# Optimization experiments

Hardware: AMD Instinct MI355X
Metric: run time of the kernel (lower is better)

Reference implementation:

```python
import jax, jax.numpy as jnp
import numpy as np

WS = 8          # window size (8x8)
HEADS = 8
DIM_HEAD = 28
SCALE = DIM_HEAD ** -0.5


def _window_partition(t, ws=WS):
    # [b, H, W, c] -> [b, n_windows, ws*ws, c]
    b, H, W, c = t.shape
    t = t.reshape(b, H // ws, ws, W // ws, ws, c)
    t = t.transpose(0, 1, 3, 2, 4, 5)
    return t.reshape(b, (H // ws) * (W // ws), ws * ws, c)


def _window_reverse(t, H, W, ws=WS):
    # [b, n_windows, ws*ws, c] -> [b, H, W, c]
    b = t.shape[0]
    c = t.shape[-1]
    t = t.reshape(b, H // ws, W // ws, ws, ws, c)
    t = t.transpose(0, 1, 3, 2, 4, 5)
    return t.reshape(b, H, W, c)


def _heads_split(t, nh):
    # [b, n, mm, (nh*d)] -> [b, n, nh, mm, d]
    b, n, mm, cd = t.shape
    return t.reshape(b, n, mm, nh, cd // nh).transpose(0, 1, 3, 2, 4)


def setup_inputs() -> dict:
    key = jax.random.key(0)
    ks = jax.random.split(key, 6)
    b, H, W, c = 128, 32, 32, 224
    inner = DIM_HEAD * HEADS  # 224
    return {
        "x": jax.random.normal(ks[0], (b, H, W, c), jnp.float32),
        "Wq": jax.random.normal(ks[1], (c, inner), jnp.float32) * (c ** -0.5),
        "Wkv": jax.random.normal(ks[2], (c, 2 * inner), jnp.float32) * (c ** -0.5),
        "Wout": jax.random.normal(ks[3], (inner, c), jnp.float32) * (inner ** -0.5),
        "bout": jnp.zeros((c,), jnp.float32),
        "pos_emb1": jax.random.normal(ks[4], (1, 1, HEADS // 2, WS * WS, WS * WS), jnp.float32),
        "pos_emb2": jax.random.normal(ks[5], (1, 1, HEADS // 2, 16, 16), jnp.float32),
    }


def reference(x, Wq, Wkv, Wout, bout, pos_emb1, pos_emb2):
    b, H, W, c = x.shape
    nh = HEADS // 2  # heads per branch

    q = x @ Wq                       # [b,H,W,224]
    kv = x @ Wkv
    k, v = jnp.split(kv, 2, axis=-1)

    half = c // 2
    q1, q2 = q[..., :half], q[..., half:]
    k1, k2 = k[..., :half], k[..., half:]
    v1, v2 = v[..., :half], v[..., half:]

    # ----- local branch: attention within each 8x8 window -----
    q1 = _heads_split(_window_partition(q1), nh) * SCALE  # [b,n,nh,64,d]
    k1 = _heads_split(_window_partition(k1), nh)
    v1 = _heads_split(_window_partition(v1), nh)
    sim1 = jnp.einsum('bnhid,bnhjd->bnhij', q1, k1) + pos_emb1
    attn1 = jax.nn.softmax(sim1, axis=-1)
    out1 = jnp.einsum('bnhij,bnhjd->bnhid', attn1, v1)    # [b,n,nh,64,d]
    bN = out1.shape[1]
    out1 = out1.transpose(0, 1, 3, 2, 4).reshape(b, bN, WS * WS, half)

    # ----- global branch: attention across windows (same in-window position) -----
    def part_global(t):
        t = _window_partition(t)                 # [b,n,mm,half]
        t = t.transpose(0, 2, 1, 3)              # [b,mm,n,half]
        return _heads_split(t, nh)               # [b,mm,nh,n,d]
    q2 = part_global(q2) * SCALE
    k2 = part_global(k2)
    v2 = part_global(v2)
    sim2 = jnp.einsum('bnhid,bnhjd->bnhij', q2, k2) + pos_emb2
    attn2 = jax.nn.softmax(sim2, axis=-1)
    out2 = jnp.einsum('bnhij,bnhjd->bnhid', attn2, v2)    # [b,mm,nh,n,d]
    out2 = out2.transpose(0, 1, 3, 2, 4).reshape(b, WS * WS, bN, half)
    out2 = out2.transpose(0, 2, 1, 3)                     # [b,n,mm,half]

    out = jnp.concatenate([out1, out2], axis=-1)          # [b,n,mm,c]
    out = out @ Wout + bout
    return _window_reverse(out, H, W)
```

## Files before the change

kernel.cpp:

```cpp
#include <hip/hip_runtime.h>
#include <stdint.h>

typedef short s8v __attribute__((ext_vector_type(8)));
typedef float f4v __attribute__((ext_vector_type(4)));
typedef unsigned short u16;

#define MFMA16(a, b, c) __builtin_amdgcn_mfma_f32_16x16x32_bf16(a, b, c, 0, 0, 0)
#define SCALE 0.1889822365046136f

__device__ __forceinline__ u16 f2bf(float f) {
  union { float f; uint32_t u; } v;
  v.f = f;
  uint32_t u = v.u;
  u += 0x7fffu + ((u >> 16) & 1u);
  return (u16)(u >> 16);
}

__device__ __forceinline__ void gld_lds16(const void* g, void* l) {
  __builtin_amdgcn_global_load_lds(
      (const __attribute__((address_space(1))) void*)g,
      (__attribute__((address_space(3))) void*)l, 16, 0, 0);
}

__global__ void prep_kernel(const float* __restrict__ Wq,
                            const float* __restrict__ Wkv,
                            const float* __restrict__ Wout,
                            u16* __restrict__ wqkvt,
                            u16* __restrict__ woutt) {
  const int gsz = gridDim.x * blockDim.x;
  const int gt = blockIdx.x * blockDim.x + threadIdx.x;
  for (int i = gt; i < 768 * 224; i += gsz) {
    const int n = i / 224, k = i - n * 224;
    float v = 0.f;
    if (n < 224) v = Wq[k * 224 + n];
    else if (n < 672) v = Wkv[k * 448 + (n - 224)];
    wqkvt[i] = f2bf(v);
  }
  for (int i = gt; i < 256 * 224; i += gsz) {
    const int n = i / 224, k = i - n * 224;
    const float v = (n < 224) ? Wout[k * 224 + n] : 0.f;
    woutt[i] = f2bf(v);
  }
}

template <int A_F32, int OUT_F32, int NTILES>
__global__ __launch_bounds__(256) void gemm_af(const void* __restrict__ Ap,
                                               const u16* __restrict__ Bt,
                                               void* __restrict__ Cp,
                                               const float* __restrict__ bias,
                                               int Nvalid, int ldc) {
  extern __shared__ u16 smem[];
  u16* As  = smem;
  u16* Bs0 = smem + 28672;
  u16* Bs1 = smem + 32768;
  const int tid = threadIdx.x;
  const int wave = tid >> 6, lane = tid & 63;
  const int c16 = lane & 15, g = lane >> 4;
  const int m0 = blockIdx.x * 128;
  const int wm = wave & 1, wn = wave >> 1;

  const int fbw = wave * 1024 + lane * 16;
  const int brow0 = fbw >> 6, bcol0 = (fbw & 63) >> 1;

#define STAGE_B(ntile, ktile, bufp)                                            \
  do {                                                                         \
    char* bb = (char*)((bufp) ? Bs1 : Bs0) + wave * 1024;                      \
    const u16* src =                                                           \
        Bt + (size_t)((ntile) * 128 + brow0) * 224 + (ktile) * 32 + bcol0;     \
    gld_lds16(src, bb);                                                        \
    gld_lds16(src + (size_t)64 * 224, bb + 4096);                              \
  } while (0)

  STAGE_B(0, 0, 0);
  if (NTILES * 7 > 1) STAGE_B(0, 1, 1);

  if (A_F32) {
    const float* Af = (const float*)Ap + (size_t)m0 * 224;
#pragma unroll
    for (int rnd = 0; rnd < 28; ++rnd) {
      const int e0 = rnd * 1024 + tid * 4;
      const float4 v = *(const float4*)(Af + e0);
      ushort4 o;
      o.x = f2bf(v.x); o.y = f2bf(v.y); o.z = f2bf(v.z); o.w = f2bf(v.w);
      *(ushort4*)(As + e0) = o;
    }
  } else {
    for (int rnd = 0; rnd < 14; ++rnd) {
      const int fb = rnd * 4096 + fbw;
      const int row = fb / 448;
      const int off = fb - row * 448;
      gld_lds16((const u16*)Ap + (size_t)(m0 + row) * 224 + (off >> 1),
                (char*)As + rnd * 4096 + wave * 1024);
    }
  }

  __syncthreads();

  for (int nt = 0; nt < NTILES; ++nt) {
    f4v acc[4][4] = {};
    for (int kt = 0; kt < 7; ++kt) {
      const int t = nt * 7 + kt;
      const u16* Bs = (t & 1) ? Bs1 : Bs0;
      s8v af[4], bf[4];
      for (int tt = 0; tt < 4; ++tt)
        af[tt] = *(const s8v*)&As[(wm * 64 + tt * 16 + c16) * 224 + kt * 32 + g * 8];
      for (int tt = 0; tt < 4; ++tt)
        bf[tt] = *(const s8v*)&Bs[(wn * 64 + tt * 16 + c16) * 32 + g * 8];
      for (int i = 0; i < 4; ++i)
        for (int j = 0; j < 4; ++j)
          acc[i][j] = MFMA16(af[i], bf[j], acc[i][j]);
      __syncthreads();
      const int ns = t + 2;
      if (ns < NTILES * 7) {
        const int nnt = ns / 7;
        STAGE_B(nnt, ns - nnt * 7, t & 1);
      }
    }
    const int n0 = nt * 128;
    for (int i = 0; i < 4; ++i) {
      const int rowb = m0 + wm * 64 + i * 16 + g * 4;
      for (int j = 0; j < 4; ++j) {
        const int col = n0 + wn * 64 + j * 16 + c16;
        if (col < Nvalid) {
          if (OUT_F32) {
            const float bz = bias[col];
            for (int r = 0; r < 4; ++r)
              ((float*)Cp)[(size_t)(rowb + r) * ldc + col] = acc[i][j][r] + bz;
          } else {
            for (int r = 0; r < 4; ++r)
              ((u16*)Cp)[(size_t)(rowb + r) * ldc + col] = f2bf(acc[i][j][r]);
          }
        }
      }
    }
  }
#undef STAGE_B
}

__device__ __forceinline__ void attn_local_body(u16* sm, int blk, int tid,
                                                const u16* __restrict__ qkv,
                                                const float* __restrict__ pos1,
                                                u16* __restrict__ attn) {
  u16* qs = sm;
  u16* ks = sm + 8192;
  u16* vt = sm + 18432;
  u16* pm = sm;
  const int b = blk >> 4, win = blk & 15;
  const int wy = win >> 2, wx = win & 3;
  const int base_s = (b * 32 + wy * 8) * 32 + wx * 8;
#pragma unroll
  for (int m = 0; m < 14; ++m) {
    const int idx = m * 256 + tid;
    const int q7 = idx / 7;
    const int c4 = idx - q7 * 7;
    const int t = q7 & 63, h = (q7 >> 6) & 3, mtx = q7 >> 8;
    const int s = base_s + (t >> 3) * 32 + (t & 7);
    const ushort4 v = *(const ushort4*)(qkv + (size_t)s * 672 + mtx * 224 + h * 28 + c4 * 4);
    *(ushort4*)((mtx ? ks : qs) + (h * 64 + t) * 32 + c4 * 4) = v;
  }
#pragma unroll
  for (int m = 0; m < 2; ++m) {
    const int idx = m * 256 + tid;
    const int mtx = idx >> 8;
    const int h = (idx >> 6) & 3, t = idx & 63;
    const ushort4 z = {0, 0, 0, 0};
    *(ushort4*)((mtx ? ks : qs) + (h * 64 + t) * 32 + 28) = z;
  }
  {
    const int t = tid & 63, wq = tid >> 6;
    const int s = base_s + (t >> 3) * 32 + (t & 7);
    const u16* vrow = qkv + (size_t)s * 672 + 448 + wq * 28;
    u16* vcolbase = vt + (wq * 32) * 72 + t;
#pragma unroll
    for (int c4 = 0; c4 < 7; ++c4) {
      const ushort4 v = *(const ushort4*)(vrow + c4 * 4);
      u16* col = vcolbase + (c4 * 4) * 72;
      col[0] = v.x; col[72] = v.y; col[144] = v.z; col[216] = v.w;
    }
  }
  __syncthreads();
  const int h = tid >> 6, lane = tid & 63;
  const int c16 = lane & 15, g = lane >> 4;
  s8v af[4], bf[4];
  for (int t = 0; t < 4; ++t) af[t] = *(const s8v*)&qs[(h * 64 + t * 16 + c16) * 32 + g * 8];
  for (int t = 0; t < 4; ++t) bf[t] = *(const s8v*)&ks[(h * 64 + t * 16 + c16) * 32 + g * 8];
  const f4v fz = {0.f, 0.f, 0.f, 0.f};
  f4v sc[4][4];
  for (int i = 0; i < 4; ++i)
    for (int j = 0; j < 4; ++j)
      sc[i][j] = MFMA16(af[i], bf[j], fz);
  float lrow[4][4];
  const float* ph = pos1 + h * 4096;
  for (int i = 0; i < 4; ++i) {
    for (int r = 0; r < 4; ++r) {
      const int irow = i * 16 + g * 4 + r;
      float mx = -1e30f;
      for (int j = 0; j < 4; ++j) {
        const float v = sc[i][j][r] * SCALE + ph[irow * 64 + j * 16 + c16];
        sc[i][j][r] = v;
        mx = fmaxf(mx, v);
      }
      for (int d = 1; d < 16; d <<= 1) mx = fmaxf(mx, __shfl_xor(mx, d, 64));
      float sum = 0.f;
      for (int j = 0; j < 4; ++j) {
        const float e = __expf(sc[i][j][r] - mx);
        sc[i][j][r] = e;
        sum += e;
      }
      for (int d = 1; d < 16; d <<= 1) sum += __shfl_xor(sum, d, 64);
      lrow[i][r] = sum;
    }
  }
  __syncthreads();
  for (int i = 0; i < 4; ++i)
    for (int r = 0; r < 4; ++r) {
      const int irow = i * 16 + g * 4 + r;
      for (int j = 0; j < 4; ++j)
        pm[(h * 64 + irow) * 72 + j * 16 + c16] = f2bf(sc[i][j][r]);
    }
  f4v o[4][2] = {};
  for (int kk = 0; kk < 2; ++kk) {
    s8v ap[4], bv[2];
    for (int t = 0; t < 4; ++t)
      ap[t] = *(const s8v*)&pm[(h * 64 + t * 16 + c16) * 72 + kk * 32 + g * 8];
    for (int t = 0; t < 2; ++t)
      bv[t] = *(const s8v*)&vt[(h * 32 + t * 16 + c16) * 72 + kk * 32 + g * 8];
    for (int i = 0; i < 4; ++i)
      for (int j = 0; j < 2; ++j)
        o[i][j] = MFMA16(ap[i], bv[j], o[i][j]);
  }
  for (int i = 0; i < 4; ++i)
    for (int r = 0; r < 4; ++r) {
      const int irow = i * 16 + g * 4 + r;
      const int s = base_s + (irow >> 3) * 32 + (irow & 7);
      const float inv = 1.f / lrow[i][r];
      for (int j = 0; j < 2; ++j) {
        const int d = j * 16 + c16;
        if (d < 28)
          attn[(size_t)s * 224 + h * 28 + d] = f2bf(o[i][j][r] * inv);
      }
    }
}

__device__ __forceinline__ void attn_global_body(u16* smg, int blk, int tid,
                                                 const u16* __restrict__ qkv,
                                                 const float* __restrict__ pos2,
                                                 u16* __restrict__ attn) {
  u16* qs = smg;
  u16* ks = smg + 8192;
  u16* vt = smg + 16384;
  u16* p2 = smg + 24608;
  const int b = blk >> 4, ig = blk & 15;
#pragma unroll
  for (int m = 0; m < 14; ++m) {
    const int idx = m * 256 + tid;
    const int q7 = idx / 7;
    const int d4 = idx - q7 * 7;
    const int hq = q7 & 3, row = (q7 >> 2) & 63, seg = q7 >> 8;
    const int w = row >> 4, j = row & 15;
    const int ii = ig * 4 + w;
    const int y = ii >> 3, x = ii & 7;
    const int s = (b * 32 + (j >> 2) * 8 + y) * 32 + (j & 3) * 8 + x;
    const ushort4 v =
        *(const ushort4*)(qkv + (size_t)s * 672 + 112 + seg * 224 + hq * 28 + d4 * 4);
    *(ushort4*)((seg ? ks : qs) + ((w * 4 + hq) * 16 + j) * 32 + hq * 0 + d4 * 4) = v;
  }
  {
    const int j = tid & 15, w = (tid >> 4) & 3, wq = tid >> 6;
    const int ii = ig * 4 + w;
    const int y = ii >> 3, x = ii & 7;
    const int s = (b * 32 + (j >> 2) * 8 + y) * 32 + (j & 3) * 8 + x;
    const u16* vrow = qkv + (size_t)s * 672 + 560;
    u16* vbase = vt + w * 2056 + j;
#pragma unroll
    for (int c4o = 0; c4o < 7; ++c4o) {
      const int c4 = c4o * 4 + wq;
      const int hq = c4 / 7;
      const int d4 = c4 - hq * 7;
      const ushort4 v = *(const ushort4*)(vrow + c4 * 4);
      u16* col = vbase + (hq * 32 + d4 * 4) * 16;
      col[0] = v.x; col[16] = v.y; col[32] = v.z; col[48] = v.w;
    }
  }
#pragma unroll
  for (int m = 0; m < 2; ++m) {
    const int idx = m * 256 + tid;
    const ushort4 z = {0, 0, 0, 0};
    *(ushort4*)(((idx & 256) ? ks : qs) + (idx & 255) * 32 + 28) = z;
  }
  {
    const ushort4 z = {0, 0, 0, 0};
    const int w = tid >> 6, hq = (tid >> 4) & 3;
    const int dd = 28 + ((tid >> 2) & 3), j4 = tid & 3;
    *(ushort4*)(vt + w * 2056 + (hq * 32 + dd) * 16 + j4 * 4) = z;
  }
  __syncthreads();
  const int w = tid >> 6, lane = tid & 63;
  const int c16 = lane & 15, g = lane >> 4;
  const int i = ig * 4 + w;
  const int y = i >> 3, x = i & 7;
  const int w4 = w * 4;
  const f4v fz = {0.f, 0.f, 0.f, 0.f};
  for (int h = 0; h < 4; ++h) {
    const s8v aq = *(const s8v*)&qs[((w4 + h) * 16 + c16) * 32 + g * 8];
    const s8v bk = *(const s8v*)&ks[((w4 + h) * 16 + c16) * 32 + g * 8];
    const f4v s = MFMA16(aq, bk, fz);
    const float* ph = pos2 + h * 256;
    float l[4];
    for (int r = 0; r < 4; ++r) {
      const float v = s[r] * SCALE + ph[(g * 4 + r) * 16 + c16];
      float mx = v;
      for (int d = 1; d < 16; d <<= 1) mx = fmaxf(mx, __shfl_xor(mx, d, 64));
      const float e = __expf(v - mx);
      float sum = e;
      for (int d = 1; d < 16; d <<= 1) sum += __shfl_xor(sum, d, 64);
      l[r] = sum;
      p2[(w * 16 + g * 4 + r) * 32 + c16] = f2bf(e);
      p2[(w * 16 + g * 4 + r) * 32 + c16 + 16] = 0;
    }
    const s8v ap = *(const s8v*)&p2[(w * 16 + c16) * 32 + g * 8];
    f4v o[2];
    for (int nt = 0; nt < 2; ++nt) {
      s8v bv = {0, 0, 0, 0, 0, 0, 0, 0};
      if (g < 2)
        bv = *(const s8v*)&vt[w * 2056 + (h * 32 + nt * 16 + c16) * 16 + g * 8];
      o[nt] = MFMA16(ap, bv, fz);
    }
    for (int nt = 0; nt < 2; ++nt)
      for (int r = 0; r < 4; ++r) {
        const int d = nt * 16 + c16;
        if (d < 28) {
          const int wi = g * 4 + r;
          const int sw = (b * 32 + (wi >> 2) * 8 + y) * 32 + (wi & 3) * 8 + x;
          attn[(size_t)sw * 224 + 112 + h * 28 + d] = f2bf(o[nt][r] / l[r]);
        }
      }
  }
}

__global__ __launch_bounds__(256) void attn_fused(const u16* __restrict__ qkv,
                                                  const float* __restrict__ pos1,
                                                  const float* __restrict__ pos2,
                                                  u16* __restrict__ attn) {
  extern __shared__ u16 sm[];
  const int blk = blockIdx.x;
  const int tid = threadIdx.x;
  if (blk < 2048)
    attn_local_body(sm, blk, tid, qkv, pos1, attn);
  else
    attn_global_body(sm, blk - 2048, tid, qkv, pos2, attn);
}

extern "C" void kernel_launch(void* const* d_in, const int* in_sizes, int n_in,
                              void* d_out, int out_size, void* d_ws, size_t ws_size,
                              hipStream_t stream) {
  const float* x    = (const float*)d_in[0];
  const float* Wq   = (const float*)d_in[1];
  const float* Wkv  = (const float*)d_in[2];
  const float* Wout = (const float*)d_in[3];
  const float* bout = (const float*)d_in[4];
  const float* pos1 = (const float*)d_in[5];
  const float* pos2 = (const float*)d_in[6];
  char* ws = (char*)d_ws;
  u16* qkv   = (u16*)ws;
  u16* attn  = (u16*)(ws + 176160768);
  u16* wqkvt = (u16*)(ws + 234881024);
  u16* woutt = (u16*)(ws + 235225088);

  prep_kernel<<<dim3(128), 256, 0, stream>>>(Wq, Wkv, Wout, wqkvt, woutt);

  gemm_af<1, 0, 6><<<dim3(1024), 256, 73728, stream>>>(x, wqkvt, qkv, nullptr, 672, 672);

  attn_fused<<<dim3(4096), 256, 55296, stream>>>(qkv, pos1, pos2, attn);

  gemm_af<0, 1, 2><<<dim3(1024), 256, 73728, stream>>>(attn, woutt, d_out, bout, 224, 224);
}
```

Baseline: 385.8 us.

## Pre-convert x to bf16 and switch GEMMs to one output tile per block

Converts x from fp32 to bf16 in a separate pass inside the prep kernel, and restructures both GEMMs so each block computes a single 128x128 output tile. A and B k-slices are double-buffered through LDS with async global-to-LDS loads, and block IDs are remapped (bid&7 interleave) so neighbouring blocks share work. This cuts LDS use from 73728 to 32768 bytes, which allows higher occupancy and more blocks, at the cost of an extra full read and write of x and reloading A once per N tile.

```diff
diff --git a/kernel.cpp b/kernel.cpp
--- a/kernel.cpp
+++ b/kernel.cpp
@@ -22,13 +22,21 @@
       (__attribute__((address_space(3))) void*)l, 16, 0, 0);
 }
 
-__global__ void prep_kernel(const float* __restrict__ Wq,
+__global__ void prep_kernel(const float4* __restrict__ x4,
+                            const float* __restrict__ Wq,
                             const float* __restrict__ Wkv,
                             const float* __restrict__ Wout,
+                            u16* __restrict__ xb,
                             u16* __restrict__ wqkvt,
                             u16* __restrict__ woutt) {
   const int gsz = gridDim.x * blockDim.x;
   const int gt = blockIdx.x * blockDim.x + threadIdx.x;
+  for (int i = gt; i < 7340032; i += gsz) {
+    float4 v = x4[i];
+    ushort4 o;
+    o.x = f2bf(v.x); o.y = f2bf(v.y); o.z = f2bf(v.z); o.w = f2bf(v.w);
+    ((ushort4*)xb)[i] = o;
+  }
   for (int i = gt; i < 768 * 224; i += gsz) {
     const int n = i / 224, k = i - n * 224;
     float v = 0.f;
@@ -43,98 +51,84 @@
   }
 }
 
-template <int A_F32, int OUT_F32, int NTILES>
-__global__ __launch_bounds__(256) void gemm_af(const void* __restrict__ Ap,
+template <int OUT_F32, int NT>
+__global__ __launch_bounds__(256) void gemm_st(const u16* __restrict__ A,
                                                const u16* __restrict__ Bt,
                                                void* __restrict__ Cp,
                                                const float* __restrict__ bias,
-                                               int Nvalid, int ldc) {
+                                               int Nvalid, int ldc, int cpx) {
   extern __shared__ u16 smem[];
-  u16* As  = smem;
-  u16* Bs0 = smem + 28672;
-  u16* Bs1 = smem + 32768;
+  u16* As0 = smem;
+  u16* As1 = smem + 4096;
+  u16* Bs0 = smem + 8192;
+  u16* Bs1 = smem + 12288;
   const int tid = threadIdx.x;
   const int wave = tid >> 6, lane = tid & 63;
   const int c16 = lane & 15, g = lane >> 4;
-  const int m0 = blockIdx.x * 128;
   const int wm = wave & 1, wn = wave >> 1;
+
+  const int bid = blockIdx.x;
+  const int work = (bid & 7) * cpx + (bid >> 3);
+  const int mt = work / NT;
+  const int nt = work - mt * NT;
+  const int m0 = mt * 128, n0 = nt * 128;
 
   const int fbw = wave * 1024 + lane * 16;
   const int brow0 = fbw >> 6, bcol0 = (fbw & 63) >> 1;
 
-#define STAGE_B(ntile, ktile, bufp)                                            \
+#define STAGE(Base, rtile, ktile, bufp)                                        \
   do {                                                                         \
-    char* bb = (char*)((bufp) ? Bs1 : Bs0) + wave * 1024;                      \
+    char* bb = (char*)(bufp) + wave * 1024;                                    \
     const u16* src =                                                           \
-        Bt + (size_t)((ntile) * 128 + brow0) * 224 + (ktile) * 32 + bcol0;     \
+        (Base) + (size_t)((rtile) * 128 + brow0) * 224 + (ktile) * 32 + bcol0; \
     gld_lds16(src, bb);                                                        \
     gld_lds16(src + (size_t)64 * 224, bb + 4096);                              \
   } while (0)
 
-  STAGE_B(0, 0, 0);
-  if (NTILES * 7 > 1) STAGE_B(0, 1, 1);
-
-  if (A_F32) {
-    const float* Af = (const float*)Ap + (size_t)m0 * 224;
-#pragma unroll
-    for (int rnd = 0; rnd < 28; ++rnd) {
-      const int e0 = rnd * 1024 + tid * 4;
-      const float4 v = *(const float4*)(Af + e0);
-      ushort4 o;
-      o.x = f2bf(v.x); o.y = f2bf(v.y); o.z = f2bf(v.z); o.w = f2bf(v.w);
-      *(ushort4*)(As + e0) = o;
-    }
-  } else {
-    for (int rnd = 0; rnd < 14; ++rnd) {
-      const int fb = rnd * 4096 + fbw;
-      const int row = fb / 448;
-      const int off = fb - row * 448;
-      gld_lds16((const u16*)Ap + (size_t)(m0 + row) * 224 + (off >> 1),
-                (char*)As + rnd * 4096 + wave * 1024);
-    }
-  }
-
+  STAGE(A, mt, 0, As0);
+  STAGE(Bt, nt, 0, Bs0);
+  STAGE(A, mt, 1, As1);
+  STAGE(Bt, nt, 1, Bs1);
   __syncthreads();
 
-  for (int nt = 0; nt < NTILES; ++nt) {
-    f4v acc[4][4] = {};
-    for (int kt = 0; kt < 7; ++kt) {
-      const int t = nt * 7 + kt;
-      const u16* Bs = (t & 1) ? Bs1 : Bs0;
-      s8v af[4], bf[4];
-      for (int tt = 0; tt < 4; ++tt)
-        af[tt] = *(const s8v*)&As[(wm * 64 + tt * 16 + c16) * 224 + kt * 32 + g * 8];
-      for (int tt = 0; tt < 4; ++tt)
-        bf[tt] = *(const s8v*)&Bs[(wn * 64 + tt * 16 + c16) * 32 + g * 8];
-      for (int i = 0; i < 4; ++i)
-        for (int j = 0; j < 4; ++j)
-          acc[i][j] = MFMA16(af[i], bf[j], acc[i][j]);
+  f4v acc[4][4] = {};
+  for (int kt = 0; kt < 7; ++kt) {
+    const u16* Asc = (kt & 1) ? As1 : As0;
+    const u16* Bsc = (kt & 1) ? Bs1 : Bs0;
+    s8v af[4], bf[4];
+    for (int tt = 0; tt < 4; ++tt)
+      af[tt] = *(const s8v*)&Asc[(wm * 64 + tt * 16 + c16) * 32 + g * 8];
+    for (int tt = 0; tt < 4; ++tt)
+      bf[tt] = *(const s8v*)&Bsc[(wn * 64 + tt * 16 + c16) * 32 + g * 8];
+    for (int i = 0; i < 4; ++i)
+      for (int j = 0; j < 4; ++j)
+        acc[i][j] = MFMA16(af[i], bf[j], acc[i][j]);
+    if (kt < 6) {
       __syncthreads();
-      const int ns = t + 2;
-      if (ns < NTILES * 7) {
-        const int nnt = ns / 7;
-        STAGE_B(nnt, ns - nnt * 7, t & 1);
-      }
-    }
-    const int n0 = nt * 128;
-    for (int i = 0; i < 4; ++i) {
-      const int rowb = m0 + wm * 64 + i * 16 + g * 4;
-      for (int j = 0; j < 4; ++j) {
-        const int col = n0 + wn * 64 + j * 16 + c16;
-        if (col < Nvalid) {
-          if (OUT_F32) {
-            const float bz = bias[col];
-            for (int r = 0; r < 4; ++r)
-              ((float*)Cp)[(size_t)(rowb + r) * ldc + col] = acc[i][j][r] + bz;
-          } else {
-            for (int r = 0; r < 4; ++r)
-              ((u16*)Cp)[(size_t)(rowb + r) * ldc + col] = f2bf(acc[i][j][r]);
-          }
+      if (kt + 2 < 7) {
+        STAGE(A, mt, kt + 2, (kt & 1) ? As1 : As0);
+        STAGE(Bt, nt, kt + 2, (kt & 1) ? Bs1 : Bs0);
+      }
+    }
+  }
+
+  for (int i = 0; i < 4; ++i) {
+    const int rowb = m0 + wm * 64 + i * 16 + g * 4;
+    for (int j = 0; j < 4; ++j) {
+      const int col = n0 + wn * 64 + j * 16 + c16;
+      if (col < Nvalid) {
+        if (OUT_F32) {
+          const float bz = bias[col];
+          for (int r = 0; r < 4; ++r)
+            ((float*)Cp)[(size_t)(rowb + r) * ldc + col] = acc[i][j][r] + bz;
+        } else {
+          for (int r = 0; r < 4; ++r)
+            ((u16*)Cp)[(size_t)(rowb + r) * ldc + col] = f2bf(acc[i][j][r]);
         }
       }
     }
   }
-#undef STAGE_B
+#undef STAGE
 }
 
 __device__ __forceinline__ void attn_local_body(u16* sm, int blk, int tid,
@@ -263,7 +257,7 @@
     const int s = (b * 32 + (j >> 2) * 8 + y) * 32 + (j & 3) * 8 + x;
     const ushort4 v =
         *(const ushort4*)(qkv + (size_t)s * 672 + 112 + seg * 224 + hq * 28 + d4 * 4);
-    *(ushort4*)((seg ? ks : qs) + ((w * 4 + hq) * 16 + j) * 32 + hq * 0 + d4 * 4) = v;
+    *(ushort4*)((seg ? ks : qs) + ((w * 4 + hq) * 16 + j) * 32 + d4 * 4) = v;
   }
   {
     const int j = tid & 15, w = (tid >> 4) & 3, wq = tid >> 6;
@@ -363,15 +357,19 @@
   const float* pos2 = (const float*)d_in[6];
   char* ws = (char*)d_ws;
   u16* qkv   = (u16*)ws;
-  u16* attn  = (u16*)(ws + 176160768);
+  u16* xb    = (u16*)(ws + 176160768);
+  u16* attn  = xb;
   u16* wqkvt = (u16*)(ws + 234881024);
   u16* woutt = (u16*)(ws + 235225088);
 
-  prep_kernel<<<dim3(128), 256, 0, stream>>>(Wq, Wkv, Wout, wqkvt, woutt);
-
-  gemm_af<1, 0, 6><<<dim3(1024), 256, 73728, stream>>>(x, wqkvt, qkv, nullptr, 672, 672);
+  prep_kernel<<<dim3(1024), 256, 0, stream>>>(
+      (const float4*)x, Wq, Wkv, Wout, xb, wqkvt, woutt);
+
+  gemm_st<0, 6><<<dim3(6144), 256, 32768, stream>>>(
+      xb, wqkvt, qkv, nullptr, 672, 672, 768);
 
   attn_fused<<<dim3(4096), 256, 55296, stream>>>(qkv, pos1, pos2, attn);
 
-  gemm_af<0, 1, 2><<<dim3(1024), 256, 73728, stream>>>(attn, woutt, d_out, bout, 224, 224);
-}
+  gemm_st<1, 2><<<dim3(2048), 256, 32768, stream>>>(
+      attn, woutt, d_out, bout, 224, 224, 256);
+}
```

Measured after the change: 418.6 us. 8.5% more time.

## Load Q fragments directly to registers and shrink attention LDS footprint

Applied to the files above, without the earlier changes.

The local and global attention bodies now load Q operands straight from global memory into MFMA fragment registers instead of staging them through shared memory. The local kernel also writes the P matrix in two halves into a narrower buffer, with extra barriers between them. Together these cut the shared-memory allocation from 55296 to 38912 bytes so more workgroups can be resident per CU. The cost is uncoalesced 8-byte global Q loads and additional __syncthreads in the P·V loop.

```diff
diff --git a/kernel.cpp b/kernel.cpp
--- a/kernel.cpp
+++ b/kernel.cpp
@@ -20,6 +20,13 @@
   __builtin_amdgcn_global_load_lds(
       (const __attribute__((address_space(1))) void*)g,
       (__attribute__((address_space(3))) void*)l, 16, 0, 0);
+}
+
+__device__ __forceinline__ s8v mk8(ushort4 lo, ushort4 hi) {
+  s8v r;
+  r[0] = (short)lo.x; r[1] = (short)lo.y; r[2] = (short)lo.z; r[3] = (short)lo.w;
+  r[4] = (short)hi.x; r[5] = (short)hi.y; r[6] = (short)hi.z; r[7] = (short)hi.w;
+  return r;
 }
 
 __global__ void prep_kernel(const float* __restrict__ Wq,
@@ -141,30 +148,42 @@
                                                 const u16* __restrict__ qkv,
                                                 const float* __restrict__ pos1,
                                                 u16* __restrict__ attn) {
-  u16* qs = sm;
-  u16* ks = sm + 8192;
-  u16* vt = sm + 18432;
   u16* pm = sm;
+  u16* ks = sm;
+  u16* vt = sm + 10240;
   const int b = blk >> 4, win = blk & 15;
   const int wy = win >> 2, wx = win & 3;
   const int base_s = (b * 32 + wy * 8) * 32 + wx * 8;
-#pragma unroll
-  for (int m = 0; m < 14; ++m) {
+  const int h = tid >> 6, lane = tid & 63;
+  const int c16 = lane & 15, g = lane >> 4;
+
+  s8v af[4];
+  {
+    const ushort4 z4 = {0, 0, 0, 0};
+#pragma unroll
+    for (int t = 0; t < 4; ++t) {
+      const int row = t * 16 + c16;
+      const int s = base_s + (row >> 3) * 32 + (row & 7);
+      const u16* qrow = qkv + (size_t)s * 672 + h * 28 + g * 8;
+      const ushort4 lo = *(const ushort4*)qrow;
+      const ushort4 hi = (g < 3) ? *(const ushort4*)(qrow + 4) : z4;
+      af[t] = mk8(lo, hi);
+    }
+  }
+#pragma unroll
+  for (int m = 0; m < 7; ++m) {
     const int idx = m * 256 + tid;
     const int q7 = idx / 7;
     const int c4 = idx - q7 * 7;
-    const int t = q7 & 63, h = (q7 >> 6) & 3, mtx = q7 >> 8;
+    const int t = q7 & 63, hh = q7 >> 6;
     const int s = base_s + (t >> 3) * 32 + (t & 7);
-    const ushort4 v = *(const ushort4*)(qkv + (size_t)s * 672 + mtx * 224 + h * 28 + c4 * 4);
-    *(ushort4*)((mtx ? ks : qs) + (h * 64 + t) * 32 + c4 * 4) = v;
-  }
-#pragma unroll
-  for (int m = 0; m < 2; ++m) {
-    const int idx = m * 256 + tid;
-    const int mtx = idx >> 8;
-    const int h = (idx >> 6) & 3, t = idx & 63;
+    const ushort4 v = *(const ushort4*)(qkv + (size_t)s * 672 + 224 + hh * 28 + c4 * 4);
+    *(ushort4*)(ks + (hh * 64 + t) * 32 + c4 * 4) = v;
+  }
+  {
+    const int hh = tid >> 6, t = tid & 63;
     const ushort4 z = {0, 0, 0, 0};
-    *(ushort4*)((mtx ? ks : qs) + (h * 64 + t) * 32 + 28) = z;
+    *(ushort4*)(ks + (hh * 64 + t) * 32 + 28) = z;
   }
   {
     const int t = tid & 63, wq = tid >> 6;
@@ -179,11 +198,10 @@
     }
   }
   __syncthreads();
-  const int h = tid >> 6, lane = tid & 63;
-  const int c16 = lane & 15, g = lane >> 4;
-  s8v af[4], bf[4];
-  for (int t = 0; t < 4; ++t) af[t] = *(const s8v*)&qs[(h * 64 + t * 16 + c16) * 32 + g * 8];
-  for (int t = 0; t < 4; ++t) bf[t] = *(const s8v*)&ks[(h * 64 + t * 16 + c16) * 32 + g * 8];
+
+  s8v bf[4];
+  for (int t = 0; t < 4; ++t)
+    bf[t] = *(const s8v*)&ks[(h * 64 + t * 16 + c16) * 32 + g * 8];
   const f4v fz = {0.f, 0.f, 0.f, 0.f};
   f4v sc[4][4];
   for (int i = 0; i < 4; ++i)
@@ -212,22 +230,26 @@
     }
   }
   __syncthreads();
-  for (int i = 0; i < 4; ++i)
-    for (int r = 0; r < 4; ++r) {
-      const int irow = i * 16 + g * 4 + r;
-      for (int j = 0; j < 4; ++j)
-        pm[(h * 64 + irow) * 72 + j * 16 + c16] = f2bf(sc[i][j][r]);
-    }
+
   f4v o[4][2] = {};
+#pragma unroll
   for (int kk = 0; kk < 2; ++kk) {
+    for (int i = 0; i < 4; ++i)
+      for (int r = 0; r < 4; ++r) {
+        const int irow = i * 16 + g * 4 + r;
+        pm[(h * 64 + irow) * 40 + c16]      = f2bf(sc[i][kk * 2][r]);
+        pm[(h * 64 + irow) * 40 + 16 + c16] = f2bf(sc[i][kk * 2 + 1][r]);
+      }
+    __syncthreads();
     s8v ap[4], bv[2];
     for (int t = 0; t < 4; ++t)
-      ap[t] = *(const s8v*)&pm[(h * 64 + t * 16 + c16) * 72 + kk * 32 + g * 8];
+      ap[t] = *(const s8v*)&pm[(h * 64 + t * 16 + c16) * 40 + g * 8];
     for (int t = 0; t < 2; ++t)
       bv[t] = *(const s8v*)&vt[(h * 32 + t * 16 + c16) * 72 + kk * 32 + g * 8];
     for (int i = 0; i < 4; ++i)
       for (int j = 0; j < 2; ++j)
         o[i][j] = MFMA16(ap[i], bv[j], o[i][j]);
+    if (kk == 0) __syncthreads();
   }
   for (int i = 0; i < 4; ++i)
     for (int r = 0; r < 4; ++r) {
@@ -246,24 +268,23 @@
                                                  const u16* __restrict__ qkv,
                                                  const float* __restrict__ pos2,
                                                  u16* __restrict__ attn) {
-  u16* qs = smg;
-  u16* ks = smg + 8192;
-  u16* vt = smg + 16384;
-  u16* p2 = smg + 24608;
+  u16* ks = smg;
+  u16* vt = smg + 8192;
+  u16* p2 = smg + 16416;
   const int b = blk >> 4, ig = blk & 15;
 #pragma unroll
-  for (int m = 0; m < 14; ++m) {
+  for (int m = 0; m < 7; ++m) {
     const int idx = m * 256 + tid;
     const int q7 = idx / 7;
     const int d4 = idx - q7 * 7;
-    const int hq = q7 & 3, row = (q7 >> 2) & 63, seg = q7 >> 8;
+    const int hq = q7 & 3, row = q7 >> 2;
     const int w = row >> 4, j = row & 15;
     const int ii = ig * 4 + w;
     const int y = ii >> 3, x = ii & 7;
     const int s = (b * 32 + (j >> 2) * 8 + y) * 32 + (j & 3) * 8 + x;
     const ushort4 v =
-        *(const ushort4*)(qkv + (size_t)s * 672 + 112 + seg * 224 + hq * 28 + d4 * 4);
-    *(ushort4*)((seg ? ks : qs) + ((w * 4 + hq) * 16 + j) * 32 + hq * 0 + d4 * 4) = v;
+        *(const ushort4*)(qkv + (size_t)s * 672 + 336 + hq * 28 + d4 * 4);
+    *(ushort4*)(ks + ((w * 4 + hq) * 16 + j) * 32 + d4 * 4) = v;
   }
   {
     const int j = tid & 15, w = (tid >> 4) & 3, wq = tid >> 6;
@@ -282,14 +303,9 @@
       col[0] = v.x; col[16] = v.y; col[32] = v.z; col[48] = v.w;
     }
   }
-#pragma unroll
-  for (int m = 0; m < 2; ++m) {
-    const int idx = m * 256 + tid;
+  {
     const ushort4 z = {0, 0, 0, 0};
-    *(ushort4*)(((idx & 256) ? ks : qs) + (idx & 255) * 32 + 28) = z;
-  }
-  {
-    const ushort4 z = {0, 0, 0, 0};
+    *(ushort4*)(ks + tid * 32 + 28) = z;
     const int w = tid >> 6, hq = (tid >> 4) & 3;
     const int dd = 28 + ((tid >> 2) & 3), j4 = tid & 3;
     *(ushort4*)(vt + w * 2056 + (hq * 32 + dd) * 16 + j4 * 4) = z;
@@ -300,9 +316,15 @@
   const int i = ig * 4 + w;
   const int y = i >> 3, x = i & 7;
   const int w4 = w * 4;
+  const int sc16 = (b * 32 + (c16 >> 2) * 8 + y) * 32 + (c16 & 3) * 8 + x;
+  const u16* rowp = qkv + (size_t)sc16 * 672;
   const f4v fz = {0.f, 0.f, 0.f, 0.f};
+  const ushort4 z4 = {0, 0, 0, 0};
   for (int h = 0; h < 4; ++h) {
-    const s8v aq = *(const s8v*)&qs[((w4 + h) * 16 + c16) * 32 + g * 8];
+    const int qo = 112 + h * 28;
+    const ushort4 qlo = *(const ushort4*)(rowp + qo + g * 8);
+    const ushort4 qhi = (g < 3) ? *(const ushort4*)(rowp + qo + g * 8 + 4) : z4;
+    const s8v aq = mk8(qlo, qhi);
     const s8v bk = *(const s8v*)&ks[((w4 + h) * 16 + c16) * 32 + g * 8];
     const f4v s = MFMA16(aq, bk, fz);
     const float* ph = pos2 + h * 256;
@@ -371,7 +393,7 @@
 
   gemm_af<1, 0, 6><<<dim3(1024), 256, 73728, stream>>>(x, wqkvt, qkv, nullptr, 672, 672);
 
-  attn_fused<<<dim3(4096), 256, 55296, stream>>>(qkv, pos1, pos2, attn);
+  attn_fused<<<dim3(4096), 256, 38912, stream>>>(qkv, pos1, pos2, attn);
 
   gemm_af<0, 1, 2><<<dim3(1024), 256, 73728, stream>>>(attn, woutt, d_out, bout, 224, 224);
 }
```

Result: slower. 395.2 us (+2.4%).
